# Kernel optimization log

Hardware: AMD Instinct MI355X
Metric: run time of the kernel (lower is better)

The kernel has to match this reference:

```python
import jax, jax.numpy as jnp
import numpy as np

N_USERS = 200000
N_ITEMS = 100000
N_EDGES = 1000000
D = 64
NUM_LAYERS = 3
BATCH = 8192


def setup_inputs() -> dict:
    key = jax.random.key(0)
    ks = jax.random.split(key, 8)
    return {
        "user_feat": jax.random.normal(ks[0], (N_USERS, D), dtype=jnp.float32) * 0.1,
        "item_feat": jax.random.normal(ks[1], (N_ITEMS, D), dtype=jnp.float32) * 0.1,
        "edge_u": jax.random.randint(ks[2], (N_EDGES,), 0, N_USERS, dtype=jnp.int32),
        "edge_i": jax.random.randint(ks[3], (N_EDGES,), 0, N_ITEMS, dtype=jnp.int32),
        "norm": jax.random.uniform(ks[4], (N_EDGES,), dtype=jnp.float32),
        "users": jax.random.randint(ks[5], (BATCH,), 0, N_USERS, dtype=jnp.int32),
        "pos_items": jax.random.randint(ks[6], (BATCH,), 0, N_ITEMS, dtype=jnp.int32),
        "neg_items": jax.random.randint(ks[7], (BATCH,), 0, N_ITEMS, dtype=jnp.int32),
    }


def reference(user_feat, item_feat, edge_u, edge_i, norm, users, pos_items, neg_items):
    # LightGCN propagation: each layer does edge-weighted gather-scatter
    # (u_mul_e 'h','norm' -> sum) in both directions of the bipartite graph.
    u_h, i_h = user_feat, item_feat
    u_acc, i_acc = u_h, i_h
    w = norm[:, None]  # [E, 1]
    for _ in range(NUM_LAYERS):
        # user -> item messages
        new_i = jax.ops.segment_sum(u_h[edge_u] * w, edge_i, num_segments=N_ITEMS)
        # item -> user messages
        new_u = jax.ops.segment_sum(i_h[edge_i] * w, edge_u, num_segments=N_USERS)
        u_h, i_h = new_u, new_i
        u_acc = u_acc + u_h
        i_acc = i_acc + i_h
    scale = 1.0 / (NUM_LAYERS + 1)
    u_acc = u_acc * scale
    i_acc = i_acc * scale
    return (u_acc[users], i_acc[pos_items], i_acc[neg_items])
```

## Files before the change

kernel.cpp:

```cpp
#include <hip/hip_runtime.h>


#define N_USERS 200000
#define N_ITEMS 100000
#define N_EDGES 1000000
#define DIM 64
#define BATCH 8192
#define NTOT (N_USERS + N_ITEMS)
#define NOUT (3 * BATCH)
#define NPART 293
#define PLOCAL 1024

#define HA 489
#define CB (NTOT * DIM / 8 / 256)
#define OB (NOUT * 16 / 256)
#define AB (NTOT / 16)
#define FB ((NOUT + 255) / 256)

__device__ __forceinline__ unsigned f2bf(float f) {
    unsigned u = __float_as_uint(f);
    return (u + 0x7fffu + ((u >> 16) & 1u)) >> 16;
}
__device__ __forceinline__ uint2 pack4(float4 v) {
    uint2 o;
    o.x = f2bf(v.x) | (f2bf(v.y) << 16);
    o.y = f2bf(v.z) | (f2bf(v.w) << 16);
    return o;
}
__device__ __forceinline__ void fma4(float4& a, uint2 v, float w) {
    a.x += __uint_as_float(v.x << 16) * w;
    a.y += __uint_as_float(v.x & 0xffff0000u) * w;
    a.z += __uint_as_float(v.y << 16) * w;
    a.w += __uint_as_float(v.y & 0xffff0000u) * w;
}
__device__ __forceinline__ int out_bucket(int orow, const int* users,
                                          const int* pos, const int* neg) {
    int seg = orow >> 13;
    int b = orow & (BATCH - 1);
    if (seg == 0) return users[b];
    if (seg == 1) return N_USERS + pos[b];
    return N_USERS + neg[b];
}

__global__ void fused_pre_kernel(const int* __restrict__ eu,
                                 const int* __restrict__ ei,
                                 int* __restrict__ partTotals,
                                 const float4* __restrict__ uf4,
                                 const float4* __restrict__ if4,
                                 unsigned short* __restrict__ F0,
                                 const float* __restrict__ u_feat,
                                 const float* __restrict__ i_feat,
                                 const int* __restrict__ users,
                                 const int* __restrict__ pos,
                                 const int* __restrict__ neg,
                                 float* __restrict__ out)
{
    __shared__ int lh[NPART];
    int bid = blockIdx.x;
    if (bid < HA) {
        for (int k = threadIdx.x; k < NPART; k += 256) lh[k] = 0;
        __syncthreads();
        int e0 = (bid * 256 + threadIdx.x) * 8;
        if (e0 < N_EDGES) {
            int4 u0 = *reinterpret_cast<const int4*>(eu + e0);
            int4 u1 = *reinterpret_cast<const int4*>(eu + e0 + 4);
            int4 i0 = *reinterpret_cast<const int4*>(ei + e0);
            int4 i1 = *reinterpret_cast<const int4*>(ei + e0 + 4);
            atomicAdd(&lh[u0.x >> 10], 1);
            atomicAdd(&lh[u0.y >> 10], 1);
            atomicAdd(&lh[u0.z >> 10], 1);
            atomicAdd(&lh[u0.w >> 10], 1);
            atomicAdd(&lh[u1.x >> 10], 1);
            atomicAdd(&lh[u1.y >> 10], 1);
            atomicAdd(&lh[u1.z >> 10], 1);
            atomicAdd(&lh[u1.w >> 10], 1);
            atomicAdd(&lh[(N_USERS + i0.x) >> 10], 1);
            atomicAdd(&lh[(N_USERS + i0.y) >> 10], 1);
            atomicAdd(&lh[(N_USERS + i0.z) >> 10], 1);
            atomicAdd(&lh[(N_USERS + i0.w) >> 10], 1);
            atomicAdd(&lh[(N_USERS + i1.x) >> 10], 1);
            atomicAdd(&lh[(N_USERS + i1.y) >> 10], 1);
            atomicAdd(&lh[(N_USERS + i1.z) >> 10], 1);
            atomicAdd(&lh[(N_USERS + i1.w) >> 10], 1);
        }
        __syncthreads();
        for (int k = threadIdx.x; k < NPART; k += 256) {
            int v = lh[k];
            if (v) atomicAdd(&partTotals[k], v);
        }
    } else if (bid < HA + CB) {
        int j = (bid - HA) * 256 + threadIdx.x;
        int f4 = j * 2;
        const int NU4 = N_USERS * DIM / 4;
        float4 a, b;
        if (f4 < NU4) { a = uf4[f4]; b = uf4[f4 + 1]; }
        else          { a = if4[f4 - NU4]; b = if4[f4 - NU4 + 1]; }
        uint2 pa = pack4(a), pb = pack4(b);
        *reinterpret_cast<uint4*>(F0 + (size_t)j * 8) =
            make_uint4(pa.x, pa.y, pb.x, pb.y);
    } else {
        int idx = (bid - HA - CB) * 256 + threadIdx.x;
        int row = idx >> 4;
        if (row >= NOUT) return;
        int d4 = (idx & 15) << 2;
        int seg = row >> 13;
        int b = row & (BATCH - 1);
        const float* src;
        if (seg == 0)      src = u_feat + (size_t)users[b] * DIM;
        else if (seg == 1) src = i_feat + (size_t)pos[b]   * DIM;
        else               src = i_feat + (size_t)neg[b]   * DIM;
        float4 v = *reinterpret_cast<const float4*>(src + d4);
        v.x *= 0.25f; v.y *= 0.25f; v.z *= 0.25f; v.w *= 0.25f;
        *reinterpret_cast<float4*>(out + (size_t)row * DIM + d4) = v;
    }
}

__global__ void part_scan_kernel(const int* __restrict__ partTotals,
                                 int* __restrict__ partStart,
                                 int* __restrict__ gcur)
{
    __shared__ int s[512];
    int t = threadIdx.x;
    s[t] = (t < NPART) ? partTotals[t] : 0;
    __syncthreads();
    for (int off = 1; off < 512; off <<= 1) {
        int x = (t >= off) ? s[t - off] : 0;
        __syncthreads();
        s[t] += x;
        __syncthreads();
    }
    if (t < NPART) {
        int st = (t == 0) ? 0 : s[t - 1];
        partStart[t] = st;
        gcur[t] = st;
    }
    if (t == NPART) partStart[NPART] = s[NPART - 1];
}

__global__ void partition_kernel(const int* __restrict__ eu,
                                 const int* __restrict__ ei,
                                 const float* __restrict__ w,
                                 int* __restrict__ gcur,
                                 uint2* __restrict__ partBuf)
{
    __shared__ int lh[NPART];
    __shared__ int lcur[NPART];
    int bid = blockIdx.x, t = threadIdx.x;
    for (int k = t; k < NPART; k += 256) lh[k] = 0;
    __syncthreads();
    int e0 = (bid * 256 + t) * 8;
    bool act = e0 < N_EDGES;
    int4 u0, u1, i0, i1;
    if (act) {
        u0 = *reinterpret_cast<const int4*>(eu + e0);
        u1 = *reinterpret_cast<const int4*>(eu + e0 + 4);
        i0 = *reinterpret_cast<const int4*>(ei + e0);
        i1 = *reinterpret_cast<const int4*>(ei + e0 + 4);
        atomicAdd(&lh[u0.x >> 10], 1);
        atomicAdd(&lh[u0.y >> 10], 1);
        atomicAdd(&lh[u0.z >> 10], 1);
        atomicAdd(&lh[u0.w >> 10], 1);
        atomicAdd(&lh[u1.x >> 10], 1);
        atomicAdd(&lh[u1.y >> 10], 1);
        atomicAdd(&lh[u1.z >> 10], 1);
        atomicAdd(&lh[u1.w >> 10], 1);
        atomicAdd(&lh[(N_USERS + i0.x) >> 10], 1);
        atomicAdd(&lh[(N_USERS + i0.y) >> 10], 1);
        atomicAdd(&lh[(N_USERS + i0.z) >> 10], 1);
        atomicAdd(&lh[(N_USERS + i0.w) >> 10], 1);
        atomicAdd(&lh[(N_USERS + i1.x) >> 10], 1);
        atomicAdd(&lh[(N_USERS + i1.y) >> 10], 1);
        atomicAdd(&lh[(N_USERS + i1.z) >> 10], 1);
        atomicAdd(&lh[(N_USERS + i1.w) >> 10], 1);
    }
    __syncthreads();
    for (int k = t; k < NPART; k += 256) {
        int v = lh[k];
        lcur[k] = v ? atomicAdd(&gcur[k], v) : 0;
    }
    __syncthreads();
    if (act) {
        float4 wa = *reinterpret_cast<const float4*>(w + e0);
        float4 wb = *reinterpret_cast<const float4*>(w + e0 + 4);
        int us[8] = {u0.x, u0.y, u0.z, u0.w, u1.x, u1.y, u1.z, u1.w};
        int is[8] = {i0.x, i0.y, i0.z, i0.w, i1.x, i1.y, i1.z, i1.w};
        float ws[8] = {wa.x, wa.y, wa.z, wa.w, wb.x, wb.y, wb.z, wb.w};
        #pragma unroll
        for (int j = 0; j < 8; ++j) {
            int bu = us[j];
            int bi = N_USERS + is[j];
            unsigned wbits = __float_as_uint(ws[j]);
            int su = atomicAdd(&lcur[bu >> 10], 1);
            partBuf[su] = make_uint2((unsigned)(bu & 1023) | ((unsigned)bi << 10), wbits);
            int si = atomicAdd(&lcur[bi >> 10], 1);
            partBuf[si] = make_uint2((unsigned)(bi & 1023) | ((unsigned)bu << 10), wbits);
        }
    }
}

__global__ void build_csr_kernel(const int* __restrict__ partStart,
                                 const uint2* __restrict__ partBuf,
                                 int* __restrict__ rp,
                                 int2* __restrict__ entries)
{
    __shared__ int h[PLOCAL];
    __shared__ int cur[PLOCAL];
    __shared__ int s[256];
    int p = blockIdx.x, t = threadIdx.x;
    int base = partStart[p], end = partStart[p + 1];
    h[t * 4 + 0] = 0; h[t * 4 + 1] = 0; h[t * 4 + 2] = 0; h[t * 4 + 3] = 0;
    __syncthreads();
    for (int r = base + t; r < end; r += 256)
        atomicAdd(&h[partBuf[r].x & 1023], 1);
    __syncthreads();
    int h0 = h[t * 4], h1 = h[t * 4 + 1], h2 = h[t * 4 + 2], h3 = h[t * 4 + 3];
    s[t] = h0 + h1 + h2 + h3;
    __syncthreads();
    for (int off = 1; off < 256; off <<= 1) {
        int x = (t >= off) ? s[t - off] : 0;
        __syncthreads();
        s[t] += x;
        __syncthreads();
    }
    int b0 = base + ((t == 0) ? 0 : s[t - 1]);
    cur[t * 4 + 0] = b0;
    cur[t * 4 + 1] = b0 + h0;
    cur[t * 4 + 2] = b0 + h0 + h1;
    cur[t * 4 + 3] = b0 + h0 + h1 + h2;
    int gb = p * PLOCAL + t * 4;
    #pragma unroll
    for (int k = 0; k < 4; ++k)
        if (gb + k <= NTOT) rp[gb + k] = cur[t * 4 + k];
    __syncthreads();
    for (int r = base + t; r < end; r += 256) {
        uint2 rec = partBuf[r];
        int b = rec.x & 1023;
        int col = rec.x >> 10;
        int slot = atomicAdd(&cur[b], 1);
        entries[slot] = make_int2(col, (int)rec.y);
    }
}

#define GATH(idx, acc)                                                        \
    {                                                                         \
        int c = __shfl(e.x, qb + (idx));                                      \
        float ww = __int_as_float(__shfl(e.y, qb + (idx)));                   \
        uint2 v = *reinterpret_cast<const uint2*>(                            \
            src + (size_t)c * DIM + l16 * 4);                                 \
        fma4(acc, v, ww);                                                     \
    }

__device__ __forceinline__ void agg_row(int row, int l16, int quad,
                                        const int* __restrict__ rp,
                                        const int2* __restrict__ entries,
                                        const unsigned short* __restrict__ src,
                                        float4& s)
{
    int beg = rp[row];
    int end = rp[row + 1];
    int cnt = end - beg;
    int qb = quad << 4;
    float4 a0 = {0,0,0,0}, a1 = {0,0,0,0}, a2 = {0,0,0,0}, a3 = {0,0,0,0};
    for (int base = 0; base < cnt; base += 16) {
        int rem = min(16, cnt - base);
        int2 e = make_int2(0, 0);
        if (l16 < rem) e = entries[beg + base + l16];
        int j = 0;
        for (; j + 7 < rem; j += 8) {
            GATH(j + 0, a0) GATH(j + 1, a1) GATH(j + 2, a2) GATH(j + 3, a3)
            GATH(j + 4, a0) GATH(j + 5, a1) GATH(j + 6, a2) GATH(j + 7, a3)
        }
        if (j + 3 < rem) {
            GATH(j + 0, a0) GATH(j + 1, a1) GATH(j + 2, a2) GATH(j + 3, a3)
            j += 4;
        }
        if (j + 1 < rem) {
            GATH(j + 0, a0) GATH(j + 1, a1)
            j += 2;
        }
        if (j < rem) GATH(j, a2)
    }
    s.x = (a0.x + a1.x) + (a2.x + a3.x);
    s.y = (a0.y + a1.y) + (a2.y + a3.y);
    s.z = (a0.z + a1.z) + (a2.z + a3.z);
    s.w = (a0.w + a1.w) + (a2.w + a3.w);
}

__global__ void agg1_flag_kernel(const int* __restrict__ rp,
                                 const int2* __restrict__ entries,
                                 const unsigned short* __restrict__ F0,
                                 unsigned short* __restrict__ H1,
                                 const int* __restrict__ users,
                                 const int* __restrict__ pos,
                                 const int* __restrict__ neg,
                                 int* __restrict__ flags)
{
    int bid = blockIdx.x;
    if (bid < AB) {
        int gid = bid * 256 + threadIdx.x;
        int lane = gid & 63;
        int quad = lane >> 4;
        int l16 = lane & 15;
        int row = (gid >> 6) * 4 + quad;
        if (row >= NTOT) return;
        float4 s;
        agg_row(row, l16, quad, rp, entries, F0, s);
        *reinterpret_cast<uint2*>(H1 + (size_t)row * DIM + l16 * 4) = pack4(s);
    } else {
        int t = (bid - AB) * 256 + threadIdx.x;
        if (t >= NOUT) return;
        int bucket = out_bucket(t, users, pos, neg);
        flags[bucket] = 1;
        int beg = rp[bucket], end = rp[bucket + 1];
        for (int k = beg; k < end; ++k)
            flags[entries[k].x] = 1;
    }
}

__global__ void compact_kernel(const int* __restrict__ flags,
                               int* __restrict__ list,
                               int* __restrict__ count)
{
    int t = blockIdx.x * blockDim.x + threadIdx.x;
    int idx = t * 4;
    if (idx >= NTOT) return;
    int4 f = *reinterpret_cast<const int4*>(flags + idx);
    int loc[4]; int k = 0;
    if (f.x) loc[k++] = idx;
    if (f.y) loc[k++] = idx + 1;
    if (f.z) loc[k++] = idx + 2;
    if (f.w) loc[k++] = idx + 3;
    if (k) {
        int base = atomicAdd(count, k);
        for (int m = 0; m < k; ++m) list[base + m] = loc[m];
    }
}

__global__ void agg2_add1_kernel(const int* __restrict__ rp,
                                 const int2* __restrict__ entries,
                                 const unsigned short* __restrict__ H1,
                                 unsigned short* __restrict__ H2,
                                 const int* __restrict__ list,
                                 const int* __restrict__ count,
                                 const int* __restrict__ users,
                                 const int* __restrict__ pos,
                                 const int* __restrict__ neg,
                                 float* __restrict__ out)
{
    int bid = blockIdx.x;
    if (bid < AB) {
        int gid = bid * 256 + threadIdx.x;
        int lane = gid & 63;
        int quad = lane >> 4;
        int l16 = lane & 15;
        int idx4 = (gid >> 6) * 4 + quad;
        int n = *count;
        if (idx4 >= n) return;
        int row = list[idx4];
        float4 s;
        agg_row(row, l16, quad, rp, entries, H1, s);
        *reinterpret_cast<uint2*>(H2 + (size_t)row * DIM + l16 * 4) = pack4(s);
    } else {
        int idx = (bid - AB) * 256 + threadIdx.x;
        int row = idx >> 4;
        if (row >= NOUT) return;
        int d4 = (idx & 15) << 2;
        int bucket = out_bucket(row, users, pos, neg);
        uint2 v = *reinterpret_cast<const uint2*>(H1 + (size_t)bucket * DIM + d4);
        float* op = out + (size_t)row * DIM + d4;
        float4 o = *reinterpret_cast<const float4*>(op);
        o.x += 0.25f * __uint_as_float(v.x << 16);
        o.y += 0.25f * __uint_as_float(v.x & 0xffff0000u);
        o.z += 0.25f * __uint_as_float(v.y << 16);
        o.w += 0.25f * __uint_as_float(v.y & 0xffff0000u);
        *reinterpret_cast<float4*>(op) = o;
    }
}

__global__ void aggout_add2_kernel(const int* __restrict__ rp,
                                   const int2* __restrict__ entries,
                                   const unsigned short* __restrict__ H2,
                                   const int* __restrict__ users,
                                   const int* __restrict__ pos,
                                   const int* __restrict__ neg,
                                   float* __restrict__ out)
{
    int gid = blockIdx.x * 256 + threadIdx.x;
    int lane = gid & 63;
    int quad = lane >> 4;
    int l16 = lane & 15;
    int orow = (gid >> 6) * 4 + quad;
    if (orow >= NOUT) return;
    int bucket = out_bucket(orow, users, pos, neg);
    float4 s;
    agg_row(bucket, l16, quad, rp, entries, H2, s);
    uint2 v = *reinterpret_cast<const uint2*>(H2 + (size_t)bucket * DIM + l16 * 4);
    s.x += __uint_as_float(v.x << 16);
    s.y += __uint_as_float(v.x & 0xffff0000u);
    s.z += __uint_as_float(v.y << 16);
    s.w += __uint_as_float(v.y & 0xffff0000u);
    float* op = out + (size_t)orow * DIM + l16 * 4;
    float4 o = *reinterpret_cast<const float4*>(op);
    o.x += 0.25f * s.x; o.y += 0.25f * s.y;
    o.z += 0.25f * s.z; o.w += 0.25f * s.w;
    *reinterpret_cast<float4*>(op) = o;
}

extern "C" void kernel_launch(void* const* d_in, const int* in_sizes, int n_in,
                              void* d_out, int out_size, void* d_ws, size_t ws_size,
                              hipStream_t stream)
{
    const float* user_feat = (const float*)d_in[0];
    const float* item_feat = (const float*)d_in[1];
    const int*   eu        = (const int*)d_in[2];
    const int*   ei        = (const int*)d_in[3];
    const float* norm      = (const float*)d_in[4];
    const int*   users     = (const int*)d_in[5];
    const int*   pos       = (const int*)d_in[6];
    const int*   neg       = (const int*)d_in[7];
    float* out = (float*)d_out;

    auto align256 = [](size_t x) { return (x + 255) & ~(size_t)255; };
    const size_t hBytes = (size_t)NTOT * DIM * sizeof(unsigned short);

    char* p = (char*)d_ws;
    unsigned short* F0 = (unsigned short*)p; p += align256(hBytes);
    unsigned short* H1 = (unsigned short*)p; p += align256(hBytes);
    unsigned short* H2 = (unsigned short*)p; p += align256(hBytes);
    int* partTotals = (int*)p; p += align256((size_t)(512 + NTOT + 16) * 4);
    int* flags = partTotals + 512;
    int* count = flags + NTOT;
    int*  partStart = (int*)p;  p += align256(512 * 4);
    int*  gcur      = (int*)p;  p += align256(512 * 4);
    int*  rp        = (int*)p;  p += align256((size_t)(NTOT + 1) * 4);
    uint2* partBuf  = (uint2*)p; p += align256((size_t)2 * N_EDGES * 8);
    int*  list      = (int*)p;  p += align256((size_t)NTOT * 4);
    int2* entries   = (int2*)p; p += align256((size_t)2 * N_EDGES * 8);

    hipMemsetAsync(partTotals, 0, (size_t)(512 + NTOT + 16) * 4, stream);

    fused_pre_kernel<<<HA + CB + OB, 256, 0, stream>>>(
        eu, ei, partTotals,
        (const float4*)user_feat, (const float4*)item_feat, F0,
        user_feat, item_feat, users, pos, neg, out);

    part_scan_kernel<<<1, 512, 0, stream>>>(partTotals, partStart, gcur);

    partition_kernel<<<HA, 256, 0, stream>>>(eu, ei, norm, gcur, partBuf);

    build_csr_kernel<<<NPART, 256, 0, stream>>>(partStart, partBuf, rp, entries);

    agg1_flag_kernel<<<AB + FB, 256, 0, stream>>>(
        rp, entries, F0, H1, users, pos, neg, flags);

    compact_kernel<<<(NTOT / 4 + 255) / 256, 256, 0, stream>>>(flags, list, count);

    agg2_add1_kernel<<<AB + OB, 256, 0, stream>>>(
        rp, entries, H1, H2, list, count, users, pos, neg, out);

    aggout_add2_kernel<<<NOUT / 16, 256, 0, stream>>>(
        rp, entries, H2, users, pos, neg, out);
}
```

Before: 312.0 us.

## Use 8 lanes per row with 16-byte gathers, widen CSR build, regroup preprocessing

The aggregation kernels now map 8 lanes to each row instead of 16, so each lane gathers 8 bf16 values with a 16-byte load and eight rows are handled per wavefront. The CSR build kernel runs 1024 threads per partition with one bin per thread, replacing four bins per thread. The feature bf16 conversion and output initialisation now run in the same launch as edge partitioning instead of alongside the histogram, leaving a histogram-only kernel first. Wider loads and more rows per wave should cut gather instruction count, at the cost of more shuffle work per lane and more serial work for high-degree rows.

New measurement: 294.1 us. 1.06x faster.

```diff
diff --git a/kernel.cpp b/kernel.cpp
--- a/kernel.cpp
+++ b/kernel.cpp
@@ -14,7 +14,7 @@
 #define HA 489
 #define CB (NTOT * DIM / 8 / 256)
 #define OB (NOUT * 16 / 256)
-#define AB (NTOT / 16)
+#define AB8 (NTOT / 32)
 #define FB ((NOUT + 255) / 256)
 
 __device__ __forceinline__ unsigned f2bf(float f) {
@@ -42,30 +42,95 @@
     return N_USERS + neg[b];
 }
 
-__global__ void fused_pre_kernel(const int* __restrict__ eu,
-                                 const int* __restrict__ ei,
-                                 int* __restrict__ partTotals,
-                                 const float4* __restrict__ uf4,
-                                 const float4* __restrict__ if4,
-                                 unsigned short* __restrict__ F0,
-                                 const float* __restrict__ u_feat,
-                                 const float* __restrict__ i_feat,
-                                 const int* __restrict__ users,
-                                 const int* __restrict__ pos,
-                                 const int* __restrict__ neg,
-                                 float* __restrict__ out)
+__global__ void hist_kernel(const int* __restrict__ eu,
+                            const int* __restrict__ ei,
+                            int* __restrict__ partTotals)
 {
     __shared__ int lh[NPART];
     int bid = blockIdx.x;
+    for (int k = threadIdx.x; k < NPART; k += 256) lh[k] = 0;
+    __syncthreads();
+    int e0 = (bid * 256 + threadIdx.x) * 8;
+    if (e0 < N_EDGES) {
+        int4 u0 = *reinterpret_cast<const int4*>(eu + e0);
+        int4 u1 = *reinterpret_cast<const int4*>(eu + e0 + 4);
+        int4 i0 = *reinterpret_cast<const int4*>(ei + e0);
+        int4 i1 = *reinterpret_cast<const int4*>(ei + e0 + 4);
+        atomicAdd(&lh[u0.x >> 10], 1);
+        atomicAdd(&lh[u0.y >> 10], 1);
+        atomicAdd(&lh[u0.z >> 10], 1);
+        atomicAdd(&lh[u0.w >> 10], 1);
+        atomicAdd(&lh[u1.x >> 10], 1);
+        atomicAdd(&lh[u1.y >> 10], 1);
+        atomicAdd(&lh[u1.z >> 10], 1);
+        atomicAdd(&lh[u1.w >> 10], 1);
+        atomicAdd(&lh[(N_USERS + i0.x) >> 10], 1);
+        atomicAdd(&lh[(N_USERS + i0.y) >> 10], 1);
+        atomicAdd(&lh[(N_USERS + i0.z) >> 10], 1);
+        atomicAdd(&lh[(N_USERS + i0.w) >> 10], 1);
+        atomicAdd(&lh[(N_USERS + i1.x) >> 10], 1);
+        atomicAdd(&lh[(N_USERS + i1.y) >> 10], 1);
+        atomicAdd(&lh[(N_USERS + i1.z) >> 10], 1);
+        atomicAdd(&lh[(N_USERS + i1.w) >> 10], 1);
+    }
+    __syncthreads();
+    for (int k = threadIdx.x; k < NPART; k += 256) {
+        int v = lh[k];
+        if (v) atomicAdd(&partTotals[k], v);
+    }
+}
+
+__global__ void part_scan_kernel(const int* __restrict__ partTotals,
+                                 int* __restrict__ partStart,
+                                 int* __restrict__ gcur)
+{
+    __shared__ int s[512];
+    int t = threadIdx.x;
+    s[t] = (t < NPART) ? partTotals[t] : 0;
+    __syncthreads();
+    for (int off = 1; off < 512; off <<= 1) {
+        int x = (t >= off) ? s[t - off] : 0;
+        __syncthreads();
+        s[t] += x;
+        __syncthreads();
+    }
+    if (t < NPART) {
+        int st = (t == 0) ? 0 : s[t - 1];
+        partStart[t] = st;
+        gcur[t] = st;
+    }
+    if (t == NPART) partStart[NPART] = s[NPART - 1];
+}
+
+__global__ void partition_conv_kernel(const int* __restrict__ eu,
+                                      const int* __restrict__ ei,
+                                      const float* __restrict__ w,
+                                      int* __restrict__ gcur,
+                                      uint2* __restrict__ partBuf,
+                                      const float4* __restrict__ uf4,
+                                      const float4* __restrict__ if4,
+                                      unsigned short* __restrict__ F0,
+                                      const float* __restrict__ u_feat,
+                                      const float* __restrict__ i_feat,
+                                      const int* __restrict__ users,
+                                      const int* __restrict__ pos,
+                                      const int* __restrict__ neg,
+                                      float* __restrict__ out)
+{
+    int bid = blockIdx.x, t = threadIdx.x;
     if (bid < HA) {
-        for (int k = threadIdx.x; k < NPART; k += 256) lh[k] = 0;
-        __syncthreads();
-        int e0 = (bid * 256 + threadIdx.x) * 8;
-        if (e0 < N_EDGES) {
-            int4 u0 = *reinterpret_cast<const int4*>(eu + e0);
-            int4 u1 = *reinterpret_cast<const int4*>(eu + e0 + 4);
-            int4 i0 = *reinterpret_cast<const int4*>(ei + e0);
-            int4 i1 = *reinterpret_cast<const int4*>(ei + e0 + 4);
+        __shared__ int lh[NPART];
+        __shared__ int lcur[NPART];
+        for (int k = t; k < NPART; k += 256) lh[k] = 0;
+        __syncthreads();
+        int e0 = (bid * 256 + t) * 8;
+        bool act = e0 < N_EDGES;
+        int4 u0, u1, i0, i1;
+        if (act) {
+            u0 = *reinterpret_cast<const int4*>(eu + e0);
+            u1 = *reinterpret_cast<const int4*>(eu + e0 + 4);
+            i0 = *reinterpret_cast<const int4*>(ei + e0);
+            i1 = *reinterpret_cast<const int4*>(ei + e0 + 4);
             atomicAdd(&lh[u0.x >> 10], 1);
             atomicAdd(&lh[u0.y >> 10], 1);
             atomicAdd(&lh[u0.z >> 10], 1);
@@ -84,12 +149,30 @@
             atomicAdd(&lh[(N_USERS + i1.w) >> 10], 1);
         }
         __syncthreads();
-        for (int k = threadIdx.x; k < NPART; k += 256) {
+        for (int k = t; k < NPART; k += 256) {
             int v = lh[k];
-            if (v) atomicAdd(&partTotals[k], v);
+            lcur[k] = v ? atomicAdd(&gcur[k], v) : 0;
+        }
+        __syncthreads();
+        if (act) {
+            float4 wa = *reinterpret_cast<const float4*>(w + e0);
+            float4 wb = *reinterpret_cast<const float4*>(w + e0 + 4);
+            int us[8] = {u0.x, u0.y, u0.z, u0.w, u1.x, u1.y, u1.z, u1.w};
+            int is[8] = {i0.x, i0.y, i0.z, i0.w, i1.x, i1.y, i1.z, i1.w};
+            float ws[8] = {wa.x, wa.y, wa.z, wa.w, wb.x, wb.y, wb.z, wb.w};
+            #pragma unroll
+            for (int j = 0; j < 8; ++j) {
+                int bu = us[j];
+                int bi = N_USERS + is[j];
+                unsigned wbits = __float_as_uint(ws[j]);
+                int su = atomicAdd(&lcur[bu >> 10], 1);
+                partBuf[su] = make_uint2((unsigned)(bu & 1023) | ((unsigned)bi << 10), wbits);
+                int si = atomicAdd(&lcur[bi >> 10], 1);
+                partBuf[si] = make_uint2((unsigned)(bi & 1023) | ((unsigned)bu << 10), wbits);
+            }
         }
     } else if (bid < HA + CB) {
-        int j = (bid - HA) * 256 + threadIdx.x;
+        int j = (bid - HA) * 256 + t;
         int f4 = j * 2;
         const int NU4 = N_USERS * DIM / 4;
         float4 a, b;
@@ -99,7 +182,7 @@
         *reinterpret_cast<uint4*>(F0 + (size_t)j * 8) =
             make_uint4(pa.x, pa.y, pb.x, pb.y);
     } else {
-        int idx = (bid - HA - CB) * 256 + threadIdx.x;
+        int idx = (bid - HA - CB) * 256 + t;
         int row = idx >> 4;
         if (row >= NOUT) return;
         int d4 = (idx & 15) << 2;
@@ -115,175 +198,82 @@
     }
 }
 
-__global__ void part_scan_kernel(const int* __restrict__ partTotals,
-                                 int* __restrict__ partStart,
-                                 int* __restrict__ gcur)
-{
-    __shared__ int s[512];
-    int t = threadIdx.x;
-    s[t] = (t < NPART) ? partTotals[t] : 0;
-    __syncthreads();
-    for (int off = 1; off < 512; off <<= 1) {
-        int x = (t >= off) ? s[t - off] : 0;
-        __syncthreads();
-        s[t] += x;
-        __syncthreads();
-    }
-    if (t < NPART) {
-        int st = (t == 0) ? 0 : s[t - 1];
-        partStart[t] = st;
-        gcur[t] = st;
-    }
-    if (t == NPART) partStart[NPART] = s[NPART - 1];
-}
-
-__global__ void partition_kernel(const int* __restrict__ eu,
-                                 const int* __restrict__ ei,
-                                 const float* __restrict__ w,
-                                 int* __restrict__ gcur,
-                                 uint2* __restrict__ partBuf)
-{
-    __shared__ int lh[NPART];
-    __shared__ int lcur[NPART];
-    int bid = blockIdx.x, t = threadIdx.x;
-    for (int k = t; k < NPART; k += 256) lh[k] = 0;
-    __syncthreads();
-    int e0 = (bid * 256 + t) * 8;
-    bool act = e0 < N_EDGES;
-    int4 u0, u1, i0, i1;
-    if (act) {
-        u0 = *reinterpret_cast<const int4*>(eu + e0);
-        u1 = *reinterpret_cast<const int4*>(eu + e0 + 4);
-        i0 = *reinterpret_cast<const int4*>(ei + e0);
-        i1 = *reinterpret_cast<const int4*>(ei + e0 + 4);
-        atomicAdd(&lh[u0.x >> 10], 1);
-        atomicAdd(&lh[u0.y >> 10], 1);
-        atomicAdd(&lh[u0.z >> 10], 1);
-        atomicAdd(&lh[u0.w >> 10], 1);
-        atomicAdd(&lh[u1.x >> 10], 1);
-        atomicAdd(&lh[u1.y >> 10], 1);
-        atomicAdd(&lh[u1.z >> 10], 1);
-        atomicAdd(&lh[u1.w >> 10], 1);
-        atomicAdd(&lh[(N_USERS + i0.x) >> 10], 1);
-        atomicAdd(&lh[(N_USERS + i0.y) >> 10], 1);
-        atomicAdd(&lh[(N_USERS + i0.z) >> 10], 1);
-        atomicAdd(&lh[(N_USERS + i0.w) >> 10], 1);
-        atomicAdd(&lh[(N_USERS + i1.x) >> 10], 1);
-        atomicAdd(&lh[(N_USERS + i1.y) >> 10], 1);
-        atomicAdd(&lh[(N_USERS + i1.z) >> 10], 1);
-        atomicAdd(&lh[(N_USERS + i1.w) >> 10], 1);
-    }
-    __syncthreads();
-    for (int k = t; k < NPART; k += 256) {
-        int v = lh[k];
-        lcur[k] = v ? atomicAdd(&gcur[k], v) : 0;
-    }
-    __syncthreads();
-    if (act) {
-        float4 wa = *reinterpret_cast<const float4*>(w + e0);
-        float4 wb = *reinterpret_cast<const float4*>(w + e0 + 4);
-        int us[8] = {u0.x, u0.y, u0.z, u0.w, u1.x, u1.y, u1.z, u1.w};
-        int is[8] = {i0.x, i0.y, i0.z, i0.w, i1.x, i1.y, i1.z, i1.w};
-        float ws[8] = {wa.x, wa.y, wa.z, wa.w, wb.x, wb.y, wb.z, wb.w};
-        #pragma unroll
-        for (int j = 0; j < 8; ++j) {
-            int bu = us[j];
-            int bi = N_USERS + is[j];
-            unsigned wbits = __float_as_uint(ws[j]);
-            int su = atomicAdd(&lcur[bu >> 10], 1);
-            partBuf[su] = make_uint2((unsigned)(bu & 1023) | ((unsigned)bi << 10), wbits);
-            int si = atomicAdd(&lcur[bi >> 10], 1);
-            partBuf[si] = make_uint2((unsigned)(bi & 1023) | ((unsigned)bu << 10), wbits);
-        }
-    }
-}
-
-__global__ void build_csr_kernel(const int* __restrict__ partStart,
-                                 const uint2* __restrict__ partBuf,
-                                 int* __restrict__ rp,
-                                 int2* __restrict__ entries)
+__global__ void __launch_bounds__(1024)
+build_csr_kernel(const int* __restrict__ partStart,
+                 const uint2* __restrict__ partBuf,
+                 int* __restrict__ rp,
+                 int2* __restrict__ entries)
 {
     __shared__ int h[PLOCAL];
+    __shared__ int s[PLOCAL];
     __shared__ int cur[PLOCAL];
-    __shared__ int s[256];
     int p = blockIdx.x, t = threadIdx.x;
     int base = partStart[p], end = partStart[p + 1];
-    h[t * 4 + 0] = 0; h[t * 4 + 1] = 0; h[t * 4 + 2] = 0; h[t * 4 + 3] = 0;
-    __syncthreads();
-    for (int r = base + t; r < end; r += 256)
+    h[t] = 0;
+    __syncthreads();
+    for (int r = base + t; r < end; r += 1024)
         atomicAdd(&h[partBuf[r].x & 1023], 1);
     __syncthreads();
-    int h0 = h[t * 4], h1 = h[t * 4 + 1], h2 = h[t * 4 + 2], h3 = h[t * 4 + 3];
-    s[t] = h0 + h1 + h2 + h3;
-    __syncthreads();
-    for (int off = 1; off < 256; off <<= 1) {
+    s[t] = h[t];
+    __syncthreads();
+    for (int off = 1; off < 1024; off <<= 1) {
         int x = (t >= off) ? s[t - off] : 0;
         __syncthreads();
         s[t] += x;
         __syncthreads();
     }
-    int b0 = base + ((t == 0) ? 0 : s[t - 1]);
-    cur[t * 4 + 0] = b0;
-    cur[t * 4 + 1] = b0 + h0;
-    cur[t * 4 + 2] = b0 + h0 + h1;
-    cur[t * 4 + 3] = b0 + h0 + h1 + h2;
-    int gb = p * PLOCAL + t * 4;
-    #pragma unroll
-    for (int k = 0; k < 4; ++k)
-        if (gb + k <= NTOT) rp[gb + k] = cur[t * 4 + k];
-    __syncthreads();
-    for (int r = base + t; r < end; r += 256) {
+    int c0 = base + s[t] - h[t];
+    cur[t] = c0;
+    int gb = p * PLOCAL + t;
+    if (gb <= NTOT) rp[gb] = c0;
+    __syncthreads();
+    for (int r = base + t; r < end; r += 1024) {
         uint2 rec = partBuf[r];
-        int b = rec.x & 1023;
-        int col = rec.x >> 10;
-        int slot = atomicAdd(&cur[b], 1);
-        entries[slot] = make_int2(col, (int)rec.y);
-    }
-}
-
-#define GATH(idx, acc)                                                        \
+        int slot = atomicAdd(&cur[rec.x & 1023], 1);
+        entries[slot] = make_int2((int)(rec.x >> 10), (int)rec.y);
+    }
+}
+
+#define GATH8(idx, aL, aH)                                                    \
     {                                                                         \
-        int c = __shfl(e.x, qb + (idx));                                      \
-        float ww = __int_as_float(__shfl(e.y, qb + (idx)));                   \
-        uint2 v = *reinterpret_cast<const uint2*>(                            \
-            src + (size_t)c * DIM + l16 * 4);                                 \
-        fma4(acc, v, ww);                                                     \
-    }
-
-__device__ __forceinline__ void agg_row(int row, int l16, int quad,
-                                        const int* __restrict__ rp,
-                                        const int2* __restrict__ entries,
-                                        const unsigned short* __restrict__ src,
-                                        float4& s)
+        int c = __shfl(e.x, gb + (idx));                                      \
+        float ww = __int_as_float(__shfl(e.y, gb + (idx)));                   \
+        uint4 v = *reinterpret_cast<const uint4*>(                            \
+            src + (size_t)c * DIM + l8 * 8);                                  \
+        fma4(aL, make_uint2(v.x, v.y), ww);                                   \
+        fma4(aH, make_uint2(v.z, v.w), ww);                                   \
+    }
+
+__device__ __forceinline__ void agg_row8(int row, int l8, int gb,
+                                         const int* __restrict__ rp,
+                                         const int2* __restrict__ entries,
+                                         const unsigned short* __restrict__ src,
+                                         float4& sL, float4& sH)
 {
     int beg = rp[row];
     int end = rp[row + 1];
     int cnt = end - beg;
-    int qb = quad << 4;
-    float4 a0 = {0,0,0,0}, a1 = {0,0,0,0}, a2 = {0,0,0,0}, a3 = {0,0,0,0};
-    for (int base = 0; base < cnt; base += 16) {
-        int rem = min(16, cnt - base);
+    float4 a0L = {0,0,0,0}, a0H = {0,0,0,0};
+    float4 a1L = {0,0,0,0}, a1H = {0,0,0,0};
+    for (int base = 0; base < cnt; base += 8) {
+        int rem = min(8, cnt - base);
         int2 e = make_int2(0, 0);
-        if (l16 < rem) e = entries[beg + base + l16];
+        if (l8 < rem) e = entries[beg + base + l8];
         int j = 0;
-        for (; j + 7 < rem; j += 8) {
-            GATH(j + 0, a0) GATH(j + 1, a1) GATH(j + 2, a2) GATH(j + 3, a3)
-            GATH(j + 4, a0) GATH(j + 5, a1) GATH(j + 6, a2) GATH(j + 7, a3)
-        }
-        if (j + 3 < rem) {
-            GATH(j + 0, a0) GATH(j + 1, a1) GATH(j + 2, a2) GATH(j + 3, a3)
-            j += 4;
+        for (; j + 3 < rem; j += 4) {
+            GATH8(j + 0, a0L, a0H) GATH8(j + 1, a1L, a1H)
+            GATH8(j + 2, a0L, a0H) GATH8(j + 3, a1L, a1H)
         }
         if (j + 1 < rem) {
-            GATH(j + 0, a0) GATH(j + 1, a1)
+            GATH8(j + 0, a0L, a0H) GATH8(j + 1, a1L, a1H)
             j += 2;
         }
-        if (j < rem) GATH(j, a2)
-    }
-    s.x = (a0.x + a1.x) + (a2.x + a3.x);
-    s.y = (a0.y + a1.y) + (a2.y + a3.y);
-    s.z = (a0.z + a1.z) + (a2.z + a3.z);
-    s.w = (a0.w + a1.w) + (a2.w + a3.w);
+        if (j < rem) GATH8(j, a0L, a0H)
+    }
+    sL.x = a0L.x + a1L.x; sL.y = a0L.y + a1L.y;
+    sL.z = a0L.z + a1L.z; sL.w = a0L.w + a1L.w;
+    sH.x = a0H.x + a1H.x; sH.y = a0H.y + a1H.y;
+    sH.z = a0H.z + a1H.z; sH.w = a0H.w + a1H.w;
 }
 
 __global__ void agg1_flag_kernel(const int* __restrict__ rp,
@@ -296,18 +286,20 @@
                                  int* __restrict__ flags)
 {
     int bid = blockIdx.x;
-    if (bid < AB) {
+    if (bid < AB8) {
         int gid = bid * 256 + threadIdx.x;
         int lane = gid & 63;
-        int quad = lane >> 4;
-        int l16 = lane & 15;
-        int row = (gid >> 6) * 4 + quad;
+        int l8 = lane & 7;
+        int gb = lane & 56;
+        int row = gid >> 3;
         if (row >= NTOT) return;
-        float4 s;
-        agg_row(row, l16, quad, rp, entries, F0, s);
-        *reinterpret_cast<uint2*>(H1 + (size_t)row * DIM + l16 * 4) = pack4(s);
+        float4 sL, sH;
+        agg_row8(row, l8, gb, rp, entries, F0, sL, sH);
+        uint2 pL = pack4(sL), pH = pack4(sH);
+        *reinterpret_cast<uint4*>(H1 + (size_t)row * DIM + l8 * 8) =
+            make_uint4(pL.x, pL.y, pH.x, pH.y);
     } else {
-        int t = (bid - AB) * 256 + threadIdx.x;
+        int t = (bid - AB8) * 256 + threadIdx.x;
         if (t >= NOUT) return;
         int bucket = out_bucket(t, users, pos, neg);
         flags[bucket] = 1;
@@ -348,20 +340,22 @@
                                  float* __restrict__ out)
 {
     int bid = blockIdx.x;
-    if (bid < AB) {
+    if (bid < AB8) {
         int gid = bid * 256 + threadIdx.x;
         int lane = gid & 63;
-        int quad = lane >> 4;
-        int l16 = lane & 15;
-        int idx4 = (gid >> 6) * 4 + quad;
+        int l8 = lane & 7;
+        int gb = lane & 56;
+        int idx = gid >> 3;
         int n = *count;
-        if (idx4 >= n) return;
-        int row = list[idx4];
-        float4 s;
-        agg_row(row, l16, quad, rp, entries, H1, s);
-        *reinterpret_cast<uint2*>(H2 + (size_t)row * DIM + l16 * 4) = pack4(s);
+        if (idx >= n) return;
+        int row = list[idx];
+        float4 sL, sH;
+        agg_row8(row, l8, gb, rp, entries, H1, sL, sH);
+        uint2 pL = pack4(sL), pH = pack4(sH);
+        *reinterpret_cast<uint4*>(H2 + (size_t)row * DIM + l8 * 8) =
+            make_uint4(pL.x, pL.y, pH.x, pH.y);
     } else {
-        int idx = (bid - AB) * 256 + threadIdx.x;
+        int idx = (bid - AB8) * 256 + threadIdx.x;
         int row = idx >> 4;
         if (row >= NOUT) return;
         int d4 = (idx & 15) << 2;
@@ -387,23 +381,31 @@
 {
     int gid = blockIdx.x * 256 + threadIdx.x;
     int lane = gid & 63;
-    int quad = lane >> 4;
-    int l16 = lane & 15;
-    int orow = (gid >> 6) * 4 + quad;
+    int l8 = lane & 7;
+    int gb = lane & 56;
+    int orow = gid >> 3;
     if (orow >= NOUT) return;
     int bucket = out_bucket(orow, users, pos, neg);
-    float4 s;
-    agg_row(bucket, l16, quad, rp, entries, H2, s);
-    uint2 v = *reinterpret_cast<const uint2*>(H2 + (size_t)bucket * DIM + l16 * 4);
-    s.x += __uint_as_float(v.x << 16);
-    s.y += __uint_as_float(v.x & 0xffff0000u);
-    s.z += __uint_as_float(v.y << 16);
-    s.w += __uint_as_float(v.y & 0xffff0000u);
-    float* op = out + (size_t)orow * DIM + l16 * 4;
-    float4 o = *reinterpret_cast<const float4*>(op);
-    o.x += 0.25f * s.x; o.y += 0.25f * s.y;
-    o.z += 0.25f * s.z; o.w += 0.25f * s.w;
-    *reinterpret_cast<float4*>(op) = o;
+    float4 sL, sH;
+    agg_row8(bucket, l8, gb, rp, entries, H2, sL, sH);
+    uint4 v = *reinterpret_cast<const uint4*>(H2 + (size_t)bucket * DIM + l8 * 8);
+    sL.x += __uint_as_float(v.x << 16);
+    sL.y += __uint_as_float(v.x & 0xffff0000u);
+    sL.z += __uint_as_float(v.y << 16);
+    sL.w += __uint_as_float(v.y & 0xffff0000u);
+    sH.x += __uint_as_float(v.z << 16);
+    sH.y += __uint_as_float(v.z & 0xffff0000u);
+    sH.z += __uint_as_float(v.w << 16);
+    sH.w += __uint_as_float(v.w & 0xffff0000u);
+    float* op = out + (size_t)orow * DIM + l8 * 8;
+    float4 o0 = *reinterpret_cast<const float4*>(op);
+    float4 o1 = *reinterpret_cast<const float4*>(op + 4);
+    o0.x += 0.25f * sL.x; o0.y += 0.25f * sL.y;
+    o0.z += 0.25f * sL.z; o0.w += 0.25f * sL.w;
+    o1.x += 0.25f * sH.x; o1.y += 0.25f * sH.y;
+    o1.z += 0.25f * sH.z; o1.w += 0.25f * sH.w;
+    *reinterpret_cast<float4*>(op) = o0;
+    *reinterpret_cast<float4*>(op + 4) = o1;
 }
 
 extern "C" void kernel_launch(void* const* d_in, const int* in_sizes, int n_in,
@@ -439,25 +441,25 @@
 
     hipMemsetAsync(partTotals, 0, (size_t)(512 + NTOT + 16) * 4, stream);
 
-    fused_pre_kernel<<<HA + CB + OB, 256, 0, stream>>>(
-        eu, ei, partTotals,
+    hist_kernel<<<HA, 256, 0, stream>>>(eu, ei, partTotals);
+
+    part_scan_kernel<<<1, 512, 0, stream>>>(partTotals, partStart, gcur);
+
+    partition_conv_kernel<<<HA + CB + OB, 256, 0, stream>>>(
+        eu, ei, norm, gcur, partBuf,
         (const float4*)user_feat, (const float4*)item_feat, F0,
         user_feat, item_feat, users, pos, neg, out);
 
-    part_scan_kernel<<<1, 512, 0, stream>>>(partTotals, partStart, gcur);
-
-    partition_kernel<<<HA, 256, 0, stream>>>(eu, ei, norm, gcur, partBuf);
-
-    build_csr_kernel<<<NPART, 256, 0, stream>>>(partStart, partBuf, rp, entries);
-
-    agg1_flag_kernel<<<AB + FB, 256, 0, stream>>>(
+    build_csr_kernel<<<NPART, 1024, 0, stream>>>(partStart, partBuf, rp, entries);
+
+    agg1_flag_kernel<<<AB8 + FB, 256, 0, stream>>>(
         rp, entries, F0, H1, users, pos, neg, flags);
 
     compact_kernel<<<(NTOT / 4 + 255) / 256, 256, 0, stream>>>(flags, list, count);
 
-    agg2_add1_kernel<<<AB + OB, 256, 0, stream>>>(
+    agg2_add1_kernel<<<AB8 + OB, 256, 0, stream>>>(
         rp, entries, H1, H2, list, count, users, pos, neg, out);
 
-    aggout_add2_kernel<<<NOUT / 16, 256, 0, stream>>>(
+    aggout_add2_kernel<<<NOUT / 32, 256, 0, stream>>>(
         rp, entries, H2, users, pos, neg, out);
 }
```
